# Optimization experiments

Measured on AMD Instinct MI355X. Metric: run time of the kernel, lower is better.

The kernel has to match this reference:

```python
import jax, jax.numpy as jnp
import numpy as np

D = 768      # embedding_dim
M = 3072     # mlp_dim
G = 4        # num_expert_groups
E = 8        # experts_per_group
KG = 2       # k_groups
KE = 4       # k_experts
EPS = 1e-6   # gate weight threshold from the torch module


def setup_inputs() -> dict:
    key = jax.random.key(0)
    ks = jax.random.split(key, 9)
    x = jax.random.normal(ks[0], (1, 1024, D), dtype=jnp.float32)
    Wg = jax.random.normal(ks[1], (D, G), dtype=jnp.float32) * 0.02
    bg = jax.random.normal(ks[2], (G,), dtype=jnp.float32) * 0.01
    We = jax.random.normal(ks[3], (G, D, E), dtype=jnp.float32) * 0.02
    be = jax.random.normal(ks[4], (G, E), dtype=jnp.float32) * 0.01
    W1 = jax.random.normal(ks[5], (G, E, D, M), dtype=jnp.float32) * 0.02
    b1 = jax.random.normal(ks[6], (G, E, M), dtype=jnp.float32) * 0.01
    W2 = jax.random.normal(ks[7], (G, E, M, D), dtype=jnp.float32) * 0.02
    b2 = jax.random.normal(ks[8], (G, E, D), dtype=jnp.float32) * 0.01
    return {"x": x, "Wg": Wg, "bg": bg, "We": We, "be": be,
            "W1": W1, "b1": b1, "W2": W2, "b2": b2}


def _topk_gates(logits, k):
    # top-k logits -> softmax over the k entries, then zero out weights < 1e-6
    top, idx = jax.lax.top_k(logits, k)
    gates = jax.nn.softmax(top, axis=-1)
    gates = jnp.where(gates >= EPS, gates, jnp.zeros_like(gates))
    return gates, idx


def reference(x, Wg, bg, We, be, W1, b1, W2, b2):
    orig_shape = x.shape
    xf = x.reshape(-1, D)  # [N, D]

    # ---- level 1: group gating (eval mode: clean logits, no noise) ----
    glog = xf @ Wg + bg                      # [N, G]
    ggates, gidx = _topk_gates(glog, KG)     # [N, KG]
    gw = jnp.einsum('nk,nkg->ng', ggates,
                    jax.nn.one_hot(gidx, G, dtype=xf.dtype))  # dense [N, G]

    # ---- level 2: expert gating within each group ----
    # computed densely for all groups; unselected groups get zero group weight
    elog = jnp.einsum('nd,gde->nge', xf, We) + be  # [N, G, E]
    egates, eidx = _topk_gates(elog, KE)            # [N, G, KE]
    ew = jnp.einsum('ngk,ngke->nge', egates,
                    jax.nn.one_hot(eidx, E, dtype=xf.dtype))  # dense [N, G, E]

    combine = gw[:, :, None] * ew  # [N, G, E] combine weights

    # ---- expert MLPs (dense compute, combine-weighted sum) ----
    y = jnp.zeros_like(xf)
    for g in range(G):  # small fixed loop over expert groups
        h = jax.nn.gelu(jnp.einsum('nd,edm->enm', xf, W1[g]) + b1[g][:, None, :],
                        approximate=False)               # [E, N, M]
        o = jnp.einsum('enm,emd->end', h, W2[g]) + b2[g][:, None, :]  # [E, N, D]
        y = y + jnp.einsum('end,ne->nd', o, combine[:, g, :])
    return y.reshape(orig_shape)
```

## Files before the change

### kernel.cpp

```cpp
#include <hip/hip_runtime.h>
#include <hip/hip_bf16.h>
#include <math.h>

#define NTOK 1024
#define DDIM 768
#define MDIM 3072
#define GN 4
#define EN 8
#define NEXP 32
#define NPAIR 8192
#define EPSW 1e-6f
#define MAXRB 64

typedef __attribute__((ext_vector_type(4))) float f32x4;
typedef __attribute__((ext_vector_type(4))) int   i32x4;
typedef __attribute__((ext_vector_type(4))) unsigned short u16x4;
typedef __attribute__((ext_vector_type(8))) __bf16 bf16x8;

__device__ __forceinline__ unsigned short f2bf(float f) {
  unsigned u = __builtin_bit_cast(unsigned, f);
  u += 0x7FFFu + ((u >> 16) & 1u);
  return (unsigned short)(u >> 16);
}

__device__ __forceinline__ void gld_lds16(const void* g, void* l) {
  __builtin_amdgcn_global_load_lds(
      (const __attribute__((address_space(1))) void*)g,
      (__attribute__((address_space(3))) void*)l, 16, 0, 0);
}

__global__ void init_kernel(int* __restrict__ p) { p[threadIdx.x] = 0; }

__global__ __launch_bounds__(256) void zero_y(float* __restrict__ y) {
  ((f32x4*)y)[blockIdx.x * 256 + threadIdx.x] = (f32x4){0.f, 0.f, 0.f, 0.f};
}

__global__ __launch_bounds__(256) void x2bf(const float* __restrict__ x,
                                            unsigned short* __restrict__ xb) {
  const int i = (blockIdx.x * 256 + threadIdx.x) * 16;
#pragma unroll
  for (int j = 0; j < 4; ++j) {
    const f32x4 v = *(const f32x4*)(x + i + j * 4);
    u16x4 p = { f2bf(v.x), f2bf(v.y), f2bf(v.z), f2bf(v.w) };
    *(u16x4*)(xb + i + j * 4) = p;
  }
}

__global__ __launch_bounds__(256) void gating_kernel(
    const float* __restrict__ x, const float* __restrict__ Wg,
    const float* __restrict__ bg, const float* __restrict__ We,
    const float* __restrict__ be, int* __restrict__ counts,
    int* __restrict__ pair_e, float* __restrict__ pair_w)
{
  __shared__ float xr[DDIM];
  __shared__ float logits[36];
  const int n = blockIdx.x;
  const int tid = threadIdx.x;
  const float* xp = x + (size_t)n * DDIM;
  for (int d = tid; d < DDIM; d += 256) xr[d] = xp[d];
  __syncthreads();

  const int w = tid >> 6, lane = tid & 63;
  for (int j = 0; j < 9; ++j) {
    const int o = w + 4 * j;
    float s = 0.f;
    if (o < 4) {
      for (int d = lane; d < DDIM; d += 64) s += xr[d] * Wg[d * GN + o];
    } else {
      const int g = (o - 4) >> 3, e = (o - 4) & 7;
      const float* wp = We + (size_t)g * DDIM * EN + e;
      for (int d = lane; d < DDIM; d += 64) s += xr[d] * wp[d * EN];
    }
    for (int off = 32; off; off >>= 1) s += __shfl_xor(s, off);
    if (lane == 0) logits[o] = s + ((o < 4) ? bg[o] : be[o - 4]);
  }
  __syncthreads();

  if (tid == 0) {
    float gl[4];
    for (int i = 0; i < 4; ++i) gl[i] = logits[i];
    int i0 = 0;
    for (int i = 1; i < 4; ++i) if (gl[i] > gl[i0]) i0 = i;
    int i1 = -1;
    for (int i = 0; i < 4; ++i) {
      if (i == i0) continue;
      if (i1 < 0 || gl[i] > gl[i1]) i1 = i;
    }
    const float m = gl[i0];
    const float e1 = expf(gl[i1] - m);
    const float s2 = 1.f + e1;
    float gv[2] = { 1.f / s2, e1 / s2 };
    int gi[2] = { i0, i1 };
    for (int r = 0; r < 2; ++r) if (gv[r] < EPSW) gv[r] = 0.f;

    for (int r = 0; r < 2; ++r) {
      const int g = gi[r];
      float el[8];
      for (int e = 0; e < 8; ++e) el[e] = logits[4 + g * 8 + e];
      int sel[4];
      for (int q = 0; q < 4; ++q) {
        int best = -1;
        for (int e = 0; e < 8; ++e) {
          bool used = false;
          for (int p = 0; p < q; ++p) if (sel[p] == e) used = true;
          if (used) continue;
          if (best < 0 || el[e] > el[best]) best = e;
        }
        sel[q] = best;
      }
      const float mm = el[sel[0]];
      float ex[4]; float ss = 0.f;
      for (int q = 0; q < 4; ++q) { ex[q] = expf(el[sel[q]] - mm); ss += ex[q]; }
      for (int q = 0; q < 4; ++q) {
        float ew = ex[q] / ss;
        if (ew < EPSW) ew = 0.f;
        const int gbl = g * 8 + sel[q];
        const int j = r * 4 + q;
        pair_e[n * 8 + j] = gbl;
        pair_w[n * 8 + j] = gv[r] * ew;
        atomicAdd(&counts[gbl], 1);
      }
    }
  }
}

__global__ void scan_kernel(const int* __restrict__ counts, int* __restrict__ offsets,
                            int* __restrict__ rb_ge, int* __restrict__ rb_by,
                            int* __restrict__ nrb)
{
  if (threadIdx.x == 0) {
    int a = 0, n = 0;
    for (int e = 0; e < NEXP; ++e) {
      offsets[e] = a;
      const int c = counts[e];
      a += c;
      for (int b = 0; b * 256 < c; ++b) { rb_ge[n] = e; rb_by[n] = b; ++n; }
    }
    *nrb = n;
  }
}

__global__ __launch_bounds__(256) void scatter_kernel(
    const int* __restrict__ pair_e, const float* __restrict__ pair_w,
    const int* __restrict__ offsets, int* __restrict__ cursor,
    int* __restrict__ slot_tok, float* __restrict__ slot_w)
{
  const int idx = blockIdx.x * 256 + threadIdx.x;
  if (idx < NPAIR) {
    const int e = pair_e[idx];
    const int s = offsets[e] + atomicAdd(&cursor[e], 1);
    slot_tok[s] = idx >> 3;
    slot_w[s] = pair_w[idx];
  }
}

template<int K, int NLD, int EPI, int GATHER, int KS>
__global__ __launch_bounds__(256, 3) void moe_gemm_bw(
    const unsigned short* __restrict__ Abase, const float* __restrict__ W,
    const float* __restrict__ bias, const int* __restrict__ counts,
    const int* __restrict__ offsets, const float* __restrict__ slot_w,
    const int* __restrict__ slot_tok, const int* __restrict__ rb_ge,
    const int* __restrict__ rb_by, const int* __restrict__ nrb,
    unsigned short* __restrict__ Hout, float* __restrict__ Yout)
{
  constexpr int KC = K / KS;
  constexpr int NT = KC / 32;
  constexpr int ABY = 16384;
  constexpr int BUFB = ABY + 4096;

  const int rb = blockIdx.x;
  if (rb >= *nrb) return;
  const int ge = rb_ge[rb];
  const int by = rb_by[rb];
  const int cnt = counts[ge];
  const int off = offsets[ge];
  const int nb = blockIdx.y;
  const int ks = (KS > 1) ? blockIdx.z : 0;
  const int kbase = ks * KC;
  const int tid = threadIdx.x;

  __shared__ __align__(16) unsigned char lds[2 * BUFB];

  const unsigned short* asrc[4];
#pragma unroll
  for (int i = 0; i < 4; ++i) {
    const int q = tid + 256 * i;
    const int m = q >> 2, c = q & 3;
    const int sc = c ^ ((m ^ (m >> 2)) & 3);
    int gr = by * 256 + m; if (gr >= cnt) gr = cnt - 1;
    const int row = GATHER ? slot_tok[off + gr] : (off + gr);
    asrc[i] = Abase + (size_t)row * K + kbase + sc * 8;
  }

  const int kq = tid >> 5, ln = tid & 31;
  const float* bp = W + (size_t)ge * K * NLD + (size_t)(kbase + kq * 4) * NLD
                      + nb * 64 + ln;
  int bwr[2];
#pragma unroll
  for (int ii = 0; ii < 2; ++ii) {
    const int n = ln + 32 * ii;
    const int s = (n ^ (n >> 2)) & 3;
    bwr[ii] = ABY + n * 64 + (((kq >> 1) ^ s) * 16) + ((kq & 1) * 8);
  }

  const int w = tid >> 6, lane = tid & 63;
  const int l15 = lane & 15, l4 = lane >> 4;
  int aoff[4], boff[4];
#pragma unroll
  for (int mf = 0; mf < 4; ++mf) {
    const int m = w * 64 + mf * 16 + l15;
    aoff[mf] = m * 64 + ((l4 ^ ((m ^ (m >> 2)) & 3)) * 16);
  }
#pragma unroll
  for (int nf = 0; nf < 4; ++nf) {
    const int n = nf * 16 + l15;
    boff[nf] = ABY + n * 64 + ((l4 ^ ((n ^ (n >> 2)) & 3)) * 16);
  }

  f32x4 acc[4][4];
#pragma unroll
  for (int mf = 0; mf < 4; ++mf)
#pragma unroll
    for (int nf = 0; nf < 4; ++nf)
      acc[mf][nf] = (f32x4){0.f, 0.f, 0.f, 0.f};

  float bA[8], bB[8];

#define ISSUE_A(T, BASE) { _Pragma("unroll") \
    for (int i = 0; i < 4; ++i) \
      gld_lds16(asrc[i] + (T) * 32, (BASE) + (tid + 256 * i) * 16); }
#define LOADB(T, BS) { _Pragma("unroll") \
    for (int ii = 0; ii < 2; ++ii) { _Pragma("unroll") \
      for (int jj = 0; jj < 4; ++jj) \
        BS[ii * 4 + jj] = bp[(size_t)((T) * 32 + jj) * NLD + 32 * ii]; } }
#define CVTW(BS, BASE) { _Pragma("unroll") \
    for (int ii = 0; ii < 2; ++ii) { \
      u16x4 p = { f2bf(BS[ii*4+0]), f2bf(BS[ii*4+1]), f2bf(BS[ii*4+2]), f2bf(BS[ii*4+3]) }; \
      *(u16x4*)((BASE) + bwr[ii]) = p; } }
#define COMPUTE(BASE) { bf16x8 afr[4], bfr[4]; _Pragma("unroll") \
    for (int mf = 0; mf < 4; ++mf) \
      afr[mf] = __builtin_bit_cast(bf16x8, *(const i32x4*)((BASE) + aoff[mf])); \
    _Pragma("unroll") \
    for (int nf = 0; nf < 4; ++nf) \
      bfr[nf] = __builtin_bit_cast(bf16x8, *(const i32x4*)((BASE) + boff[nf])); \
    _Pragma("unroll") \
    for (int mf = 0; mf < 4; ++mf) { _Pragma("unroll") \
      for (int nf = 0; nf < 4; ++nf) \
        acc[mf][nf] = __builtin_amdgcn_mfma_f32_16x16x32_bf16( \
            afr[mf], bfr[nf], acc[mf][nf], 0, 0, 0); } }
#define STEP(T, CB, IB, BASE, OBASE) { \
    CVTW(CB, BASE); \
    asm volatile("s_waitcnt lgkmcnt(0)" ::: "memory"); \
    __builtin_amdgcn_s_barrier(); \
    asm volatile("" ::: "memory"); \
    if ((T) + 1 < NT) { \
      ISSUE_A((T) + 1, OBASE); \
      __builtin_amdgcn_sched_barrier(0); \
      LOADB((T) + 1, IB); \
    } \
    COMPUTE(BASE); \
  }

  ISSUE_A(0, lds);
  __builtin_amdgcn_sched_barrier(0);
  LOADB(0, bA);

  for (int t = 0; t < NT; t += 2) {
    STEP(t,     bA, bB, lds,        lds + BUFB);
    STEP(t + 1, bB, bA, lds + BUFB, lds);
  }
#undef ISSUE_A
#undef LOADB
#undef CVTW
#undef COMPUTE
#undef STEP

#pragma unroll
  for (int mf = 0; mf < 4; ++mf) {
    const int rb2 = by * 256 + w * 64 + mf * 16 + l4 * 4;
    if constexpr (EPI == 0) {
#pragma unroll
      for (int nf = 0; nf < 4; ++nf) {
        const int col = nb * 64 + nf * 16 + l15;
        const float bv = bias[(size_t)ge * NLD + col];
#pragma unroll
        for (int j = 0; j < 4; ++j) {
          const int r = rb2 + j;
          if (r < cnt) {
            const float v = acc[mf][nf][j] + bv;
            const float gl = 0.5f * v * (1.f + erff(v * 0.70710678118654752f));
            Hout[(size_t)(off + r) * NLD + col] = f2bf(gl);
          }
        }
      }
    } else {
#pragma unroll
      for (int j = 0; j < 4; ++j) {
        const int r = rb2 + j;
        if (r < cnt) {
          const int slot = off + r;
          const float sw = slot_w[slot];
          const int tok = slot_tok[slot];
#pragma unroll
          for (int nf = 0; nf < 4; ++nf) {
            const int col = nb * 64 + nf * 16 + l15;
            const float bv = (ks == 0) ? bias[(size_t)ge * NLD + col] : 0.f;
            atomicAdd(&Yout[(size_t)tok * DDIM + col], sw * (acc[mf][nf][j] + bv));
          }
        }
      }
    }
  }
}

extern "C" void kernel_launch(void* const* d_in, const int* in_sizes, int n_in,
                              void* d_out, int out_size, void* d_ws, size_t ws_size,
                              hipStream_t stream)
{
  const float* x  = (const float*)d_in[0];
  const float* Wg = (const float*)d_in[1];
  const float* bg = (const float*)d_in[2];
  const float* We = (const float*)d_in[3];
  const float* be = (const float*)d_in[4];
  const float* W1 = (const float*)d_in[5];
  const float* b1 = (const float*)d_in[6];
  const float* W2 = (const float*)d_in[7];
  const float* b2 = (const float*)d_in[8];
  float* y = (float*)d_out;

  char* ws = (char*)d_ws;
  int*   counts   = (int*)(ws + 0);
  int*   offsets  = (int*)(ws + 128);
  int*   cursor   = (int*)(ws + 256);
  int*   nrb      = (int*)(ws + 384);
  int*   rb_ge    = (int*)(ws + 512);
  int*   rb_by    = (int*)(ws + 896);
  int*   pair_e   = (int*)(ws + 2048);
  float* pair_w   = (float*)(ws + 34816);
  int*   slot_tok = (int*)(ws + 67584);
  float* slot_w   = (float*)(ws + 100352);
  unsigned short* xb = (unsigned short*)(ws + 135168);
  unsigned short* H  = (unsigned short*)(ws + 12715008);

  init_kernel<<<1, 256, 0, stream>>>((int*)ws);
  zero_y<<<NTOK * DDIM / 1024, 256, 0, stream>>>(y);
  x2bf<<<NTOK * DDIM / 4096, 256, 0, stream>>>(x, xb);
  gating_kernel<<<NTOK, 256, 0, stream>>>(x, Wg, bg, We, be, counts, pair_e, pair_w);
  scan_kernel<<<1, 64, 0, stream>>>(counts, offsets, rb_ge, rb_by, nrb);
  scatter_kernel<<<NPAIR / 256, 256, 0, stream>>>(pair_e, pair_w, offsets, cursor,
                                                  slot_tok, slot_w);

  moe_gemm_bw<DDIM, MDIM, 0, 1, 1><<<dim3(MAXRB, MDIM / 64, 1), 256, 0, stream>>>(
      xb, W1, b1, counts, offsets, nullptr, slot_tok, rb_ge, rb_by, nrb, H, nullptr);
  moe_gemm_bw<MDIM, DDIM, 1, 0, 2><<<dim3(MAXRB, DDIM / 64, 2), 256, 0, stream>>>(
      H, W2, b2, counts, offsets, slot_w, slot_tok, rb_ge, rb_by, nrb, nullptr, y);
}
```

Baseline: 589.7 us.

## Reshape MoE GEMM tiles to 128x128 and stage fp32 weights via LDS DMA

The MoE expert GEMMs change from 256x64 tiles to 128x128 tiles, with a 2x2 wave layout. Row blocks per expert are now 128 rows, so MAXRB grows. The fp32 weight tile is loaded asynchronously into LDS with global_load_lds instead of through registers. It is then converted to bf16 with packed v_cvt_pk_bf16 and transposed in LDS. The aim is to reuse each fp32 weight read across more columns and to cut register-path load latency. The cost is an extra barrier per k-step, more LDS per block, and lower occupancy (launch bound 2).

```diff
diff --git a/kernel.cpp b/kernel.cpp
--- a/kernel.cpp
+++ b/kernel.cpp
@@ -10,7 +10,7 @@
 #define NEXP 32
 #define NPAIR 8192
 #define EPSW 1e-6f
-#define MAXRB 64
+#define MAXRB 96
 
 typedef __attribute__((ext_vector_type(4))) float f32x4;
 typedef __attribute__((ext_vector_type(4))) int   i32x4;
@@ -21,6 +21,12 @@
   unsigned u = __builtin_bit_cast(unsigned, f);
   u += 0x7FFFu + ((u >> 16) & 1u);
   return (unsigned short)(u >> 16);
+}
+
+__device__ __forceinline__ unsigned cvt_pk_bf16(float lo, float hi) {
+  unsigned r;
+  asm volatile("v_cvt_pk_bf16_f32 %0, %1, %2" : "=v"(r) : "v"(lo), "v"(hi));
+  return r;
 }
 
 __device__ __forceinline__ void gld_lds16(const void* g, void* l) {
@@ -134,7 +140,7 @@
       offsets[e] = a;
       const int c = counts[e];
       a += c;
-      for (int b = 0; b * 256 < c; ++b) { rb_ge[n] = e; rb_by[n] = b; ++n; }
+      for (int b = 0; b * 128 < c; ++b) { rb_ge[n] = e; rb_by[n] = b; ++n; }
     }
     *nrb = n;
   }
@@ -155,7 +161,7 @@
 }
 
 template<int K, int NLD, int EPI, int GATHER, int KS>
-__global__ __launch_bounds__(256, 3) void moe_gemm_bw(
+__global__ __launch_bounds__(256, 2) void moe_gemm_gl(
     const unsigned short* __restrict__ Abase, const float* __restrict__ W,
     const float* __restrict__ bias, const int* __restrict__ counts,
     const int* __restrict__ offsets, const float* __restrict__ slot_w,
@@ -165,8 +171,10 @@
 {
   constexpr int KC = K / KS;
   constexpr int NT = KC / 32;
-  constexpr int ABY = 16384;
-  constexpr int BUFB = ABY + 4096;
+  constexpr int ABY = 8192;
+  constexpr int FBY = 16384;
+  constexpr int BBY = 8192;
+  constexpr int BUFB = ABY + FBY + BBY;
 
   const int rb = blockIdx.x;
   if (rb >= *nrb) return;
@@ -181,40 +189,42 @@
 
   __shared__ __align__(16) unsigned char lds[2 * BUFB];
 
-  const unsigned short* asrc[4];
-#pragma unroll
-  for (int i = 0; i < 4; ++i) {
+  const unsigned short* asrc[2];
+#pragma unroll
+  for (int i = 0; i < 2; ++i) {
     const int q = tid + 256 * i;
     const int m = q >> 2, c = q & 3;
     const int sc = c ^ ((m ^ (m >> 2)) & 3);
-    int gr = by * 256 + m; if (gr >= cnt) gr = cnt - 1;
+    int gr = by * 128 + m; if (gr >= cnt) gr = cnt - 1;
     const int row = GATHER ? slot_tok[off + gr] : (off + gr);
     asrc[i] = Abase + (size_t)row * K + kbase + sc * 8;
   }
 
-  const int kq = tid >> 5, ln = tid & 31;
-  const float* bp = W + (size_t)ge * K * NLD + (size_t)(kbase + kq * 4) * NLD
-                      + nb * 64 + ln;
-  int bwr[2];
-#pragma unroll
-  for (int ii = 0; ii < 2; ++ii) {
-    const int n = ln + 32 * ii;
-    const int s = (n ^ (n >> 2)) & 3;
-    bwr[ii] = ABY + n * 64 + (((kq >> 1) ^ s) * 16) + ((kq & 1) * 8);
-  }
+  const float* fsrc[4];
+#pragma unroll
+  for (int i = 0; i < 4; ++i) {
+    const int q = tid + 256 * i;
+    fsrc[i] = W + (size_t)ge * K * NLD + (size_t)(kbase + (q >> 5)) * NLD
+                + nb * 128 + (q & 31) * 4;
+  }
+
+  const int tn = tid & 127;
+  const int tk0 = (tid >> 7) * 16;
+  const int tsn = (tn ^ (tn >> 2)) & 3;
 
   const int w = tid >> 6, lane = tid & 63;
+  const int wr = (w >> 1) * 64, wc = (w & 1) * 64;
   const int l15 = lane & 15, l4 = lane >> 4;
   int aoff[4], boff[4];
 #pragma unroll
   for (int mf = 0; mf < 4; ++mf) {
-    const int m = w * 64 + mf * 16 + l15;
+    const int m = wr + mf * 16 + l15;
     aoff[mf] = m * 64 + ((l4 ^ ((m ^ (m >> 2)) & 3)) * 16);
   }
 #pragma unroll
   for (int nf = 0; nf < 4; ++nf) {
-    const int n = nf * 16 + l15;
-    boff[nf] = ABY + n * 64 + ((l4 ^ ((n ^ (n >> 2)) & 3)) * 16);
+    const int n = wc + nf * 16 + l15;
+    boff[nf] = ABY + FBY + n * 64 + ((l4 ^ ((n ^ (n >> 2)) & 3)) * 16);
   }
 
   f32x4 acc[4][4];
@@ -224,19 +234,24 @@
     for (int nf = 0; nf < 4; ++nf)
       acc[mf][nf] = (f32x4){0.f, 0.f, 0.f, 0.f};
 
-  float bA[8], bB[8];
-
-#define ISSUE_A(T, BASE) { _Pragma("unroll") \
+#define ISSUE(T, BASE) { \
+    _Pragma("unroll") \
+    for (int i = 0; i < 2; ++i) \
+      gld_lds16(asrc[i] + (size_t)(T) * 32, (BASE) + (tid + 256 * i) * 16); \
+    _Pragma("unroll") \
     for (int i = 0; i < 4; ++i) \
-      gld_lds16(asrc[i] + (T) * 32, (BASE) + (tid + 256 * i) * 16); }
-#define LOADB(T, BS) { _Pragma("unroll") \
-    for (int ii = 0; ii < 2; ++ii) { _Pragma("unroll") \
-      for (int jj = 0; jj < 4; ++jj) \
-        BS[ii * 4 + jj] = bp[(size_t)((T) * 32 + jj) * NLD + 32 * ii]; } }
-#define CVTW(BS, BASE) { _Pragma("unroll") \
-    for (int ii = 0; ii < 2; ++ii) { \
-      u16x4 p = { f2bf(BS[ii*4+0]), f2bf(BS[ii*4+1]), f2bf(BS[ii*4+2]), f2bf(BS[ii*4+3]) }; \
-      *(u16x4*)((BASE) + bwr[ii]) = p; } }
+      gld_lds16(fsrc[i] + (size_t)(T) * 32 * NLD, (BASE) + ABY + (tid + 256 * i) * 16); }
+#define TRANS(BASE) { \
+    const float* fp = (const float*)((BASE) + ABY); \
+    unsigned char* bb = (BASE) + ABY + FBY; \
+    float fv[16]; \
+    _Pragma("unroll") \
+    for (int j = 0; j < 16; ++j) fv[j] = fp[(tk0 + j) * 128 + tn]; \
+    _Pragma("unroll") \
+    for (int jp = 0; jp < 8; ++jp) { \
+      const unsigned wv = cvt_pk_bf16(fv[2 * jp], fv[2 * jp + 1]); \
+      const int c = (tk0 * 2 + 4 * jp) >> 4; \
+      *(unsigned*)(bb + tn * 64 + ((c ^ tsn) * 16) + ((4 * jp) & 15)) = wv; } }
 #define COMPUTE(BASE) { bf16x8 afr[4], bfr[4]; _Pragma("unroll") \
     for (int mf = 0; mf < 4; ++mf) \
       afr[mf] = __builtin_bit_cast(bf16x8, *(const i32x4*)((BASE) + aoff[mf])); \
@@ -248,40 +263,33 @@
       for (int nf = 0; nf < 4; ++nf) \
         acc[mf][nf] = __builtin_amdgcn_mfma_f32_16x16x32_bf16( \
             afr[mf], bfr[nf], acc[mf][nf], 0, 0, 0); } }
-#define STEP(T, CB, IB, BASE, OBASE) { \
-    CVTW(CB, BASE); \
-    asm volatile("s_waitcnt lgkmcnt(0)" ::: "memory"); \
-    __builtin_amdgcn_s_barrier(); \
-    asm volatile("" ::: "memory"); \
-    if ((T) + 1 < NT) { \
-      ISSUE_A((T) + 1, OBASE); \
-      __builtin_amdgcn_sched_barrier(0); \
-      LOADB((T) + 1, IB); \
-    } \
-    COMPUTE(BASE); \
-  }
-
-  ISSUE_A(0, lds);
-  __builtin_amdgcn_sched_barrier(0);
-  LOADB(0, bA);
-
-  for (int t = 0; t < NT; t += 2) {
-    STEP(t,     bA, bB, lds,        lds + BUFB);
-    STEP(t + 1, bB, bA, lds + BUFB, lds);
-  }
-#undef ISSUE_A
-#undef LOADB
-#undef CVTW
+
+  ISSUE(0, lds);
+
+  for (int t = 0; t < NT; ++t) {
+    unsigned char* buf = lds + (t & 1) * BUFB;
+    unsigned char* obuf = lds + ((t + 1) & 1) * BUFB;
+    asm volatile("s_waitcnt vmcnt(0)" ::: "memory");
+    __builtin_amdgcn_s_barrier();
+    asm volatile("" ::: "memory");
+    if (t + 1 < NT) ISSUE(t + 1, obuf);
+    TRANS(buf);
+    asm volatile("s_waitcnt lgkmcnt(0)" ::: "memory");
+    __builtin_amdgcn_s_barrier();
+    asm volatile("" ::: "memory");
+    COMPUTE(buf);
+  }
+#undef ISSUE
+#undef TRANS
 #undef COMPUTE
-#undef STEP
 
 #pragma unroll
   for (int mf = 0; mf < 4; ++mf) {
-    const int rb2 = by * 256 + w * 64 + mf * 16 + l4 * 4;
+    const int rb2 = by * 128 + wr + mf * 16 + l4 * 4;
     if constexpr (EPI == 0) {
 #pragma unroll
       for (int nf = 0; nf < 4; ++nf) {
-        const int col = nb * 64 + nf * 16 + l15;
+        const int col = nb * 128 + wc + nf * 16 + l15;
         const float bv = bias[(size_t)ge * NLD + col];
 #pragma unroll
         for (int j = 0; j < 4; ++j) {
@@ -303,7 +311,7 @@
           const int tok = slot_tok[slot];
 #pragma unroll
           for (int nf = 0; nf < 4; ++nf) {
-            const int col = nb * 64 + nf * 16 + l15;
+            const int col = nb * 128 + wc + nf * 16 + l15;
             const float bv = (ks == 0) ? bias[(size_t)ge * NLD + col] : 0.f;
             atomicAdd(&Yout[(size_t)tok * DDIM + col], sw * (acc[mf][nf][j] + bv));
           }
@@ -350,8 +358,8 @@
   scatter_kernel<<<NPAIR / 256, 256, 0, stream>>>(pair_e, pair_w, offsets, cursor,
                                                   slot_tok, slot_w);
 
-  moe_gemm_bw<DDIM, MDIM, 0, 1, 1><<<dim3(MAXRB, MDIM / 64, 1), 256, 0, stream>>>(
+  moe_gemm_gl<DDIM, MDIM, 0, 1, 1><<<dim3(MAXRB, MDIM / 128, 1), 256, 0, stream>>>(
       xb, W1, b1, counts, offsets, nullptr, slot_tok, rb_ge, rb_by, nrb, H, nullptr);
-  moe_gemm_bw<MDIM, DDIM, 1, 0, 2><<<dim3(MAXRB, DDIM / 64, 2), 256, 0, stream>>>(
+  moe_gemm_gl<MDIM, DDIM, 1, 0, 2><<<dim3(MAXRB, DDIM / 128, 2), 256, 0, stream>>>(
       H, W2, b2, counts, offsets, slot_w, slot_tok, rb_ge, rb_by, nrb, nullptr, y);
 }
```

Result: faster. 562.1 us (-4.7%).
